# Performance work log

Hardware: AMD Instinct MI355X
Metric: run time of the kernel (lower is better)

The kernel has to match this reference:

```python
import math
import jax, jax.numpy as jnp
import numpy as np

N_NODES = 50000
N_EDGES = 600000
IN_CH = 64      # in_channels == out_channels (residual requires it)
HEADS = 2
C = 64          # per-head dim == out_channels
HC = HEADS * C  # 128
EDGE_DIM = 32


def setup_inputs() -> dict:
    key = jax.random.key(0)
    ks = jax.random.split(key, 12)
    s = 0.05
    return {
        "x": jax.random.normal(ks[0], (N_NODES, IN_CH), jnp.float32),
        "edge_index": jax.random.randint(ks[1], (2, N_EDGES), 0, N_NODES, dtype=jnp.int64),
        "edge_attr": jax.random.normal(ks[2], (N_EDGES, EDGE_DIM), jnp.float32),
        "Wq": s * jax.random.normal(ks[3], (IN_CH, HC), jnp.float32),
        "bq": jnp.zeros((HC,), jnp.float32),
        "Wk": s * jax.random.normal(ks[4], (IN_CH, HC), jnp.float32),
        "bk": jnp.zeros((HC,), jnp.float32),
        "Wv": s * jax.random.normal(ks[5], (IN_CH, HC), jnp.float32),
        "bv": jnp.zeros((HC,), jnp.float32),
        "We": s * jax.random.normal(ks[6], (EDGE_DIM, HC), jnp.float32),
        "Wp": s * jax.random.normal(ks[7], (HC, IN_CH), jnp.float32),
        "bp": jnp.zeros((IN_CH,), jnp.float32),
        "ln1_g": jnp.ones((IN_CH,), jnp.float32),
        "ln1_b": jnp.zeros((IN_CH,), jnp.float32),
        "ln2_g": jnp.ones((IN_CH,), jnp.float32),
        "ln2_b": jnp.zeros((IN_CH,), jnp.float32),
        "W1": s * jax.random.normal(ks[8], (IN_CH, IN_CH), jnp.float32),
        "b1": jnp.zeros((IN_CH,), jnp.float32),
        "W2": s * jax.random.normal(ks[9], (IN_CH, IN_CH), jnp.float32),
        "b2": jnp.zeros((IN_CH,), jnp.float32),
    }


def _layernorm(x, g, b, eps=1e-5):
    m = jnp.mean(x, axis=-1, keepdims=True)
    v = jnp.mean(jnp.square(x - m), axis=-1, keepdims=True)
    return (x - m) / jnp.sqrt(v + eps) * g + b


def reference(x, edge_index, edge_attr, Wq, bq, Wk, bk, Wv, bv, We, Wp, bp,
              ln1_g, ln1_b, ln2_g, ln2_b, W1, b1, W2, b2):
    n = x.shape[0]
    residual = x
    h = _layernorm(x, ln1_g, ln1_b)
    q = (h @ Wq + bq).reshape(n, HEADS, C)
    k = (h @ Wk + bk).reshape(n, HEADS, C)
    v = (h @ Wv + bv).reshape(n, HEADS, C)

    src, tgt = edge_index[0], edge_index[1]
    e = (edge_attr @ We).reshape(-1, HEADS, C)   # (E,H,C)
    qi = q[tgt]                                  # (E,H,C) gather by target
    kj = k[src] + e
    vj = v[src] + e

    alpha = jnp.sum(qi * kj, axis=-1) / math.sqrt(C)            # (E,H)
    amax = jax.ops.segment_max(alpha, tgt, num_segments=n)      # (N,H)
    ex = jnp.exp(alpha - amax[tgt])
    den = jax.ops.segment_sum(ex, tgt, num_segments=n)          # (N,H)
    a = ex / (den[tgt] + 1e-8)                                  # (E,H)

    agg = jax.ops.segment_sum(a[:, :, None] * vj, tgt, num_segments=n)  # (N,H,C)
    out = agg.reshape(n, HC) @ Wp + bp
    out = out + residual                        # in_channels == out_channels

    res2 = out
    o = _layernorm(out, ln2_g, ln2_b)
    o = jax.nn.gelu(o @ W1 + b1, approximate=False) @ W2 + b2
    return o + res2
```

## Files before the change

### kernel.cpp

```cpp
#include <hip/hip_runtime.h>
#include <math.h>
#include <stdint.h>


typedef float f32x4 __attribute__((ext_vector_type(4)));
typedef __bf16 bf16x8 __attribute__((ext_vector_type(8)));
typedef unsigned int u32x4 __attribute__((ext_vector_type(4)));

#define WPM_S 200
#define W1_OFF 12800
#define W2_OFF 18432
#define W_TOT 24064
#define H_S 72

__device__ __forceinline__ unsigned pack_bf16(float2 v) {
    unsigned a = __builtin_bit_cast(unsigned, v.x);
    unsigned b = __builtin_bit_cast(unsigned, v.y);
    a = (a + 0x7FFFu + ((a >> 16) & 1u)) >> 16;
    b = (b + 0x7FFFu + ((b >> 16) & 1u)) >> 16;
    return a | (b << 16);
}
__device__ __forceinline__ float2 unpack_bf16(unsigned p) {
    float x = __builtin_bit_cast(float, p << 16);
    float y = __builtin_bit_cast(float, p & 0xFFFF0000u);
    return make_float2(x, y);
}
__device__ __forceinline__ unsigned short bf16r(float x) {
    unsigned u = __builtin_bit_cast(unsigned, x);
    return (unsigned short)((u + 0x7FFFu + ((u >> 16) & 1u)) >> 16);
}

__device__ __forceinline__ f32x4 mfma16(bf16x8 a, bf16x8 b, f32x4 c) {
    return __builtin_amdgcn_mfma_f32_16x16x32_bf16(a, b, c, 0, 0, 0);
}
__device__ __forceinline__ bf16x8 frag_ld(const unsigned short* p) {
    return __builtin_bit_cast(bf16x8, *(const u32x4*)p);
}

__global__ void k_pre(const float* __restrict__ Wq, const float* __restrict__ Wk,
                      const float* __restrict__ Wv, const float* __restrict__ We,
                      const float* __restrict__ Wp, const float* __restrict__ W1,
                      const float* __restrict__ W2, const float* __restrict__ bq,
                      const float* __restrict__ bk, const float* __restrict__ bv,
                      float* __restrict__ Wqt, float* __restrict__ Wkt,
                      float* __restrict__ Wvt,
                      unsigned short* __restrict__ wsW, float* __restrict__ bqt,
                      float* __restrict__ bkt, float* __restrict__ bvt,
                      int* __restrict__ deg, int n) {
    int idx = blockIdx.x * 256 + threadIdx.x;
    for (int i = idx; i < n; i += gridDim.x * 256) deg[i] = 0;
    if (idx < 8192) {
        int cin = idx >> 7, j = idx & 127, h = j >> 6, c = j & 63;
        int dst = cin * 128 + c * 2 + h;
        Wqt[dst] = Wq[idx];
        Wkt[dst] = Wk[idx];
        Wvt[dst] = Wv[idx];
        int o = idx >> 7, k = idx & 127;
        wsW[o * WPM_S + k] = bf16r(Wp[((k & 1) * 64 + (k >> 1)) * 64 + o]);
    }
    if (idx < 4096) {
        int o = idx >> 6, k = idx & 63;
        wsW[W1_OFF + o * 88 + k] = bf16r(W1[k * 64 + o]);
        wsW[W2_OFF + o * 88 + k] = bf16r(W2[k * 64 + o]);
        int o2 = idx & 63, dh = idx >> 6, d = dh >> 1, h = dh & 1;
        float s = 0.f;
        for (int c = 0; c < 64; ++c)
            s += We[d * 128 + h * 64 + c] * Wp[(h * 64 + c) * 64 + o2];
        wsW[o2 * WPM_S + 128 + dh] = bf16r(s);
    }
    if (idx < 128) {
        int h = idx >> 6, c = idx & 63;
        bqt[c * 2 + h] = bq[idx];
        bkt[c * 2 + h] = bk[idx];
        bvt[c * 2 + h] = bv[idx];
    }
}

__global__ __launch_bounds__(256) void k_bucket(
    const int* __restrict__ ei, int* __restrict__ deg,
    int* __restrict__ bucket_e, unsigned short* __restrict__ bucket_s,
    int E, int n) {
    int e = blockIdx.x * 256 + threadIdx.x;
    if (e >= E) return;
    int src = ei[e], tgt = ei[E + e];
    src = min(max(src, 0), n - 1);
    tgt = min(max(tgt, 0), n - 1);
    int slot = atomicAdd(&deg[tgt], 1);
    if (slot < 64) {
        bucket_e[(size_t)tgt * 64 + slot] = e;
        bucket_s[(size_t)tgt * 64 + slot] = (unsigned short)src;
    }
}

__global__ __launch_bounds__(256) void k_qkv(
    const float* __restrict__ x,
    const float* __restrict__ Wqt, const float* __restrict__ Wkt, const float* __restrict__ Wvt,
    const float* __restrict__ bqt, const float* __restrict__ bkt, const float* __restrict__ bvt,
    const float* __restrict__ g1, const float* __restrict__ b1,
    const float* __restrict__ We,
    unsigned* __restrict__ qx, unsigned* __restrict__ kbf,
    unsigned* __restrict__ vbf, int n) {
    __shared__ __align__(16) float hT[4][64][8];
    __shared__ __align__(16) float qs[4][2][8][64];
    int wave = threadIdx.x >> 6, lane = threadIdx.x & 63;
    int node0 = blockIdx.x * 32 + wave * 8;
    if (node0 >= n) return;

    int b = lane >> 3, t = lane & 7;
    int nodeb = node0 + b;
    float4 xa = make_float4(0.f, 0.f, 0.f, 0.f), xb = xa;
    if (nodeb < n) {
        const float4* xp = (const float4*)(x + (size_t)nodeb * 64 + t * 8);
        xa = xp[0]; xb = xp[1];
    }
    float s1 = (xa.x + xa.y) + (xa.z + xa.w) + (xb.x + xb.y) + (xb.z + xb.w);
    float s2 = xa.x*xa.x + xa.y*xa.y + xa.z*xa.z + xa.w*xa.w
             + xb.x*xb.x + xb.y*xb.y + xb.z*xb.z + xb.w*xb.w;
#pragma unroll
    for (int m = 1; m < 8; m <<= 1) {
        s1 += __shfl_xor(s1, m);
        s2 += __shfl_xor(s2, m);
    }
    float mean = s1 * 0.015625f;
    float var  = s2 * 0.015625f - mean * mean;
    float rstd = rsqrtf(var + 1e-5f);
    float4 ga = ((const float4*)(g1 + t * 8))[0];
    float4 gb = ((const float4*)(g1 + t * 8))[1];
    float4 ba = ((const float4*)(b1 + t * 8))[0];
    float4 bb = ((const float4*)(b1 + t * 8))[1];
    float hv[8];
    hv[0] = (xa.x - mean) * rstd * ga.x + ba.x;
    hv[1] = (xa.y - mean) * rstd * ga.y + ba.y;
    hv[2] = (xa.z - mean) * rstd * ga.z + ba.z;
    hv[3] = (xa.w - mean) * rstd * ga.w + ba.w;
    hv[4] = (xb.x - mean) * rstd * gb.x + bb.x;
    hv[5] = (xb.y - mean) * rstd * gb.y + bb.y;
    hv[6] = (xb.z - mean) * rstd * gb.z + bb.z;
    hv[7] = (xb.w - mean) * rstd * gb.w + bb.w;
#pragma unroll
    for (int j = 0; j < 8; ++j) hT[wave][t * 8 + j][b] = hv[j];

    const float2* Wq2 = (const float2*)Wqt;
    const float2* Wk2 = (const float2*)Wkt;
    const float2* Wv2 = (const float2*)Wvt;
    float2 bqv = ((const float2*)bqt)[lane];
    float2 bkv = ((const float2*)bkt)[lane];
    float2 bvv = ((const float2*)bvt)[lane];
    float2 qa[8], ka[8], va[8];
#pragma unroll
    for (int nb = 0; nb < 8; ++nb) { qa[nb] = bqv; ka[nb] = bkv; va[nb] = bvv; }

#pragma unroll 4
    for (int cin = 0; cin < 64; ++cin) {
        float2 w_q = Wq2[cin * 64 + lane];
        float2 w_k = Wk2[cin * 64 + lane];
        float2 w_v = Wv2[cin * 64 + lane];
        const float4* hp = (const float4*)&hT[wave][cin][0];
        float4 h0 = hp[0], h1 = hp[1];
        float hs[8] = {h0.x, h0.y, h0.z, h0.w, h1.x, h1.y, h1.z, h1.w};
#pragma unroll
        for (int nb = 0; nb < 8; ++nb) {
            qa[nb].x += hs[nb] * w_q.x; qa[nb].y += hs[nb] * w_q.y;
            ka[nb].x += hs[nb] * w_k.x; ka[nb].y += hs[nb] * w_k.y;
            va[nb].x += hs[nb] * w_v.x; va[nb].y += hs[nb] * w_v.y;
        }
    }

#pragma unroll
    for (int nb = 0; nb < 8; ++nb) {
        int nd = node0 + nb;
        if (nd < n) {
            qx[(size_t)nd * 128 + lane] = pack_bf16(qa[nb]);
            kbf[(size_t)nd * 64 + lane] = pack_bf16(ka[nb]);
            vbf[(size_t)nd * 64 + lane] = pack_bf16(va[nb]);
        }
        qs[wave][0][nb][lane] = qa[nb].x;
        qs[wave][1][nb][lane] = qa[nb].y;
    }

    int hh = lane >> 5, d = lane & 31;
    const float4* Wr = (const float4*)(We + d * 128 + hh * 64);
    float wqa[8] = {0.f, 0.f, 0.f, 0.f, 0.f, 0.f, 0.f, 0.f};
#pragma unroll 4
    for (int c4 = 0; c4 < 16; ++c4) {
        float4 w = Wr[c4];
#pragma unroll
        for (int nb = 0; nb < 8; ++nb) {
            float4 qv = *(const float4*)&qs[wave][hh][nb][c4 * 4];
            wqa[nb] += w.x * qv.x + w.y * qv.y + w.z * qv.z + w.w * qv.w;
        }
    }
#pragma unroll
    for (int nb = 0; nb < 8; ++nb)
        if (node0 + nb < n)
            ((float*)qx)[(size_t)(node0 + nb) * 128 + 64 + d * 2 + hh] = wqa[nb];
}

__global__ __launch_bounds__(256) void k_attn(
    const unsigned* __restrict__ qx, const unsigned* __restrict__ kbf,
    const unsigned* __restrict__ vbf, const float* __restrict__ edge_attr,
    const int* __restrict__ deg, const int* __restrict__ bucket_e,
    const unsigned short* __restrict__ bucket_s,
    unsigned* __restrict__ aggs, int n, int E) {
    int wave = threadIdx.x >> 6, lane = threadIdx.x & 63;
    int node = blockIdx.x * 4 + wave;
    if (node >= n) return;
    int sub = lane >> 4, l = lane & 15;

    uint4 qq = ((const uint4*)qx)[(size_t)node * 32 + l];
    float4 w4 = ((const float4*)qx)[(size_t)node * 32 + 16 + l];
    float2 q0 = unpack_bf16(qq.x), q1 = unpack_bf16(qq.y),
           q2 = unpack_bf16(qq.z), q3 = unpack_bf16(qq.w);

    int dcount = min(deg[node], 64);
    int eid_l = 0, src_l = 0;
    if (lane < dcount) {
        eid_l = min(max(bucket_e[(size_t)node * 64 + lane], 0), E - 1);
        src_l = min((int)bucket_s[(size_t)node * 64 + lane], n - 1);
    }

    const uint4* kb4 = (const uint4*)kbf;
    const uint4* vb4 = (const uint4*)vbf;
    const float2* ea2 = (const float2*)edge_attr;

    float accA[4] = {0.f, 0.f, 0.f, 0.f}, accB[4] = {0.f, 0.f, 0.f, 0.f};
    float aS0 = 0.f, aS1 = 0.f, bS0 = 0.f, bS1 = 0.f;
    float den0 = 0.f, den1 = 0.f;

    uint4 kk, vv; float2 a2;
    {
        int jj = sub & 63;
        int ej = __shfl(eid_l, jj), sj = __shfl(src_l, jj);
        kk = kb4[(size_t)sj * 16 + l];
        vv = vb4[(size_t)sj * 16 + l];
        a2 = ea2[(size_t)ej * 16 + l];
    }
    for (int i = 0; i < dcount; i += 4) {
        uint4 kc = kk, vc = vv; float2 ac = a2;
        bool valid = (i + sub) < dcount;
        int inx = i + 4;
        if (inx < dcount) {
            int jj = (inx + sub) & 63;
            int ej = __shfl(eid_l, jj), sj = __shfl(src_l, jj);
            kk = kb4[(size_t)sj * 16 + l];
            vv = vb4[(size_t)sj * 16 + l];
            a2 = ea2[(size_t)ej * 16 + l];
        }
        float2 k0 = unpack_bf16(kc.x), k1 = unpack_bf16(kc.y),
               k2 = unpack_bf16(kc.z), k3 = unpack_bf16(kc.w);
        float r0 = q0.x * k0.x + q1.x * k1.x + q2.x * k2.x + q3.x * k3.x
                 + w4.x * ac.x + w4.z * ac.y;
        float r1 = q0.y * k0.y + q1.y * k1.y + q2.y * k2.y + q3.y * k3.y
                 + w4.y * ac.x + w4.w * ac.y;
#pragma unroll
        for (int m = 1; m < 16; m <<= 1) {
            r0 += __shfl_xor(r0, m);
            r1 += __shfl_xor(r1, m);
        }
        float ex0 = valid ? __expf(r0 * 0.125f) : 0.f;
        float ex1 = valid ? __expf(r1 * 0.125f) : 0.f;
        float2 v0 = unpack_bf16(vc.x), v1 = unpack_bf16(vc.y),
               v2 = unpack_bf16(vc.z), v3 = unpack_bf16(vc.w);
        accA[0] += ex0 * v0.x; accB[0] += ex1 * v0.y;
        accA[1] += ex0 * v1.x; accB[1] += ex1 * v1.y;
        accA[2] += ex0 * v2.x; accB[2] += ex1 * v2.y;
        accA[3] += ex0 * v3.x; accB[3] += ex1 * v3.y;
        aS0 += ex0 * ac.x; aS1 += ex1 * ac.x;
        bS0 += ex0 * ac.y; bS1 += ex1 * ac.y;
        den0 += ex0; den1 += ex1;
    }

#pragma unroll
    for (int m = 16; m < 64; m <<= 1) {
#pragma unroll
        for (int j = 0; j < 4; ++j) {
            accA[j] += __shfl_xor(accA[j], m);
            accB[j] += __shfl_xor(accB[j], m);
        }
        aS0 += __shfl_xor(aS0, m); aS1 += __shfl_xor(aS1, m);
        bS0 += __shfl_xor(bS0, m); bS1 += __shfl_xor(bS1, m);
        den0 += __shfl_xor(den0, m); den1 += __shfl_xor(den1, m);
    }

    float r0 = 1.0f / (den0 + 1e-8f);
    float r1 = 1.0f / (den1 + 1e-8f);

    float va = sub == 0 ? accA[0] : sub == 1 ? accA[1] : sub == 2 ? accA[2] : accA[3];
    float vb = sub == 0 ? accB[0] : sub == 1 ? accB[1] : sub == 2 ? accB[2] : accB[3];
    aggs[(size_t)node * 96 + 4 * l + sub] =
        pack_bf16(make_float2(va * r0, vb * r1));

    if (sub == 0) {
        unsigned s0 = pack_bf16(make_float2(aS0 * r0, aS1 * r1));
        unsigned s1 = pack_bf16(make_float2(bS0 * r0, bS1 * r1));
        *(uint2*)&aggs[(size_t)node * 96 + 64 + 2 * l] = make_uint2(s0, s1);
    }
}

__global__ __launch_bounds__(256) void k_post(
    const unsigned short* __restrict__ aggsb,
    const unsigned short* __restrict__ wsW,
    const float* __restrict__ bp, const float* __restrict__ x,
    const float* __restrict__ g2, const float* __restrict__ b2,
    const float* __restrict__ b1f, const float* __restrict__ b2f,
    float* __restrict__ out, int n) {
    __shared__ __align__(16) unsigned short sW[W_TOT];
    __shared__ __align__(16) unsigned short hb[4][2][16 * H_S];
    int tid = threadIdx.x;
    for (int i = tid; i < W_TOT / 8; i += 256)
        ((u32x4*)sW)[i] = ((const u32x4*)wsW)[i];
    __syncthreads();

    int wave = tid >> 6, lane = tid & 63;
    int cl = lane & 15, kg = lane >> 4;
    unsigned short* h2 = hb[wave][0];
    unsigned short* h3 = hb[wave][1];

    float bp_c[4], g2_c[4], b2_c[4], b1_c[4], bf2_c[4];
#pragma unroll
    for (int t = 0; t < 4; ++t) {
        int c = t * 16 + cl;
        bp_c[t] = bp[c];
        g2_c[t] = g2[c];
        b2_c[t] = b2[c];
        b1_c[t] = b1f[c];
        bf2_c[t] = b2f[c];
    }

    int wid = blockIdx.x * 4 + wave;
    int nbatch = (n + 15) >> 4;
    int nwaves = gridDim.x * 4;
    for (int bt = wid; bt < nbatch; bt += nwaves) {
        int node0 = bt * 16;

        f32x4 acc1[4];
#pragma unroll
        for (int t = 0; t < 4; ++t) acc1[t] = (f32x4){0.f, 0.f, 0.f, 0.f};
        int arow = min(node0 + cl, n - 1);
#pragma unroll
        for (int s = 0; s < 6; ++s) {
            bf16x8 af = frag_ld(aggsb + (size_t)arow * 192 + s * 32 + kg * 8);
#pragma unroll
            for (int t = 0; t < 4; ++t) {
                bf16x8 bf = frag_ld(sW + (t * 16 + cl) * WPM_S + s * 32 + kg * 8);
                acc1[t] = mfma16(af, bf, acc1[t]);
            }
        }
#pragma unroll
        for (int t = 0; t < 4; ++t) {
#pragma unroll
            for (int j = 0; j < 4; ++j) {
                int nd = min(node0 + kg * 4 + j, n - 1);
                acc1[t][j] += bp_c[t] + x[(size_t)nd * 64 + t * 16 + cl];
            }
        }

        float mean[4], rstd[4];
#pragma unroll
        for (int j = 0; j < 4; ++j) {
            float s1 = acc1[0][j] + acc1[1][j] + acc1[2][j] + acc1[3][j];
            float s2 = acc1[0][j] * acc1[0][j] + acc1[1][j] * acc1[1][j]
                     + acc1[2][j] * acc1[2][j] + acc1[3][j] * acc1[3][j];
#pragma unroll
            for (int m = 1; m < 16; m <<= 1) {
                s1 += __shfl_xor(s1, m);
                s2 += __shfl_xor(s2, m);
            }
            mean[j] = s1 * 0.015625f;
            float var = s2 * 0.015625f - mean[j] * mean[j];
            rstd[j] = rsqrtf(var + 1e-5f);
        }
#pragma unroll
        for (int t = 0; t < 4; ++t)
#pragma unroll
            for (int j = 0; j < 4; ++j) {
                float v = (acc1[t][j] - mean[j]) * rstd[j] * g2_c[t] + b2_c[t];
                h2[(kg * 4 + j) * H_S + t * 16 + cl] = bf16r(v);
            }
        asm volatile("s_waitcnt lgkmcnt(0)" ::: "memory");

        f32x4 acc2[4];
#pragma unroll
        for (int t = 0; t < 4; ++t)
            acc2[t] = (f32x4){b1_c[t], b1_c[t], b1_c[t], b1_c[t]};
#pragma unroll
        for (int s = 0; s < 2; ++s) {
            bf16x8 af = frag_ld(h2 + cl * H_S + s * 32 + kg * 8);
#pragma unroll
            for (int t = 0; t < 4; ++t) {
                bf16x8 bf = frag_ld(sW + W1_OFF + (t * 16 + cl) * 88 + s * 32 + kg * 8);
                acc2[t] = mfma16(af, bf, acc2[t]);
            }
        }
#pragma unroll
        for (int t = 0; t < 4; ++t)
#pragma unroll
            for (int j = 0; j < 4; ++j) {
                float v = acc2[t][j];
                v = 0.5f * v * (1.0f + erff(v * 0.70710678118654752f));
                h3[(kg * 4 + j) * H_S + t * 16 + cl] = bf16r(v);
            }
        asm volatile("s_waitcnt lgkmcnt(0)" ::: "memory");

        f32x4 acc3[4];
#pragma unroll
        for (int t = 0; t < 4; ++t) {
            acc3[t] = acc1[t];
#pragma unroll
            for (int j = 0; j < 4; ++j) acc3[t][j] += bf2_c[t];
        }
#pragma unroll
        for (int s = 0; s < 2; ++s) {
            bf16x8 af = frag_ld(h3 + cl * H_S + s * 32 + kg * 8);
#pragma unroll
            for (int t = 0; t < 4; ++t) {
                bf16x8 bf = frag_ld(sW + W2_OFF + (t * 16 + cl) * 88 + s * 32 + kg * 8);
                acc3[t] = mfma16(af, bf, acc3[t]);
            }
        }
#pragma unroll
        for (int t = 0; t < 4; ++t)
#pragma unroll
            for (int j = 0; j < 4; ++j) {
                int r = node0 + kg * 4 + j;
                if (r < n) out[(size_t)r * 64 + t * 16 + cl] = acc3[t][j];
            }
    }
}

extern "C" void kernel_launch(void* const* d_in, const int* in_sizes, int n_in,
                              void* d_out, int out_size, void* d_ws, size_t ws_size,
                              hipStream_t stream) {
    const float* x  = (const float*)d_in[0];
    const int*   ei = (const int*)d_in[1];
    const float* ea = (const float*)d_in[2];
    const float* Wq = (const float*)d_in[3];
    const float* bq = (const float*)d_in[4];
    const float* Wk = (const float*)d_in[5];
    const float* bk = (const float*)d_in[6];
    const float* Wv = (const float*)d_in[7];
    const float* bv = (const float*)d_in[8];
    const float* We = (const float*)d_in[9];
    const float* Wp = (const float*)d_in[10];
    const float* bp = (const float*)d_in[11];
    const float* g1 = (const float*)d_in[12];
    const float* b1 = (const float*)d_in[13];
    const float* g2 = (const float*)d_in[14];
    const float* b2 = (const float*)d_in[15];
    const float* W1 = (const float*)d_in[16];
    const float* b1f = (const float*)d_in[17];
    const float* W2 = (const float*)d_in[18];
    const float* b2f = (const float*)d_in[19];

    const int n = in_sizes[0] / 64;
    const int E = in_sizes[2] / 32;

    char* p = (char*)d_ws;
    unsigned* qx = (unsigned*)p; p += (size_t)n * 128 * 4;
    unsigned* kbf = (unsigned*)p; p += (size_t)n * 64 * 4;
    unsigned* vbf = (unsigned*)p; p += (size_t)n * 64 * 4;
    int* deg   = (int*)p;   p += (size_t)n * 4;
    p = (char*)(((uintptr_t)p + 15) & ~(uintptr_t)15);
    int* bucket_e = (int*)p; p += (size_t)n * 64 * 4;
    unsigned short* bucket_s = (unsigned short*)p; p += (size_t)n * 64 * 2;
    p = (char*)(((uintptr_t)p + 15) & ~(uintptr_t)15);
    unsigned* aggs = (unsigned*)p; p += (size_t)n * 96 * 4;
    float* Wqt = (float*)p; p += 8192 * 4;
    float* Wkt = (float*)p; p += 8192 * 4;
    float* Wvt = (float*)p; p += 8192 * 4;
    unsigned short* wsW = (unsigned short*)p; p += W_TOT * 2;
    float* bqt = (float*)p; p += 128 * 4;
    float* bkt = (float*)p; p += 128 * 4;
    float* bvt = (float*)p; p += 128 * 4;

    k_pre<<<196, 256, 0, stream>>>(Wq, Wk, Wv, We, Wp, W1, W2, bq, bk, bv,
                                   Wqt, Wkt, Wvt, wsW, bqt, bkt, bvt,
                                   deg, n);
    k_bucket<<<(E + 255) / 256, 256, 0, stream>>>(ei, deg, bucket_e, bucket_s,
                                                  E, n);
    k_qkv<<<(n + 31) / 32, 256, 0, stream>>>(x, Wqt, Wkt, Wvt, bqt, bkt, bvt,
                                             g1, b1, We, qx, kbf, vbf, n);
    k_attn<<<(n + 3) / 4, 256, 0, stream>>>(qx, kbf, vbf, ea, deg,
                                            bucket_e, bucket_s, aggs, n, E);
    int nb16 = (n + 15) >> 4;
    int blocks = (nb16 + 3) / 4;
    if (blocks > 391) blocks = 391;
    k_post<<<blocks, 256, 0, stream>>>((const unsigned short*)aggs, wsW,
                                       bp, x, g2, b2, b1f, b2f,
                                       (float*)d_out, n);
}
```

Baseline: 325.8 us.

## Compute fused QKV and Q·We projection with bf16 MFMA from LDS weights

Replaces the fp32 scalar-FMA QKV projection in k_qkv with bf16 MFMA 16x16x32 instructions. The weights are staged once per block into shared memory as a concatenated transposed bf16 matrix. The Q·We^T product is folded algebraically into a precomputed weight block (Wq·We^T plus its bias), so the second LDS pass is gone. The aim is to cut ALU time in the projection. In exchange it adds a roughly 64KB LDS weight load per block and bf16 rounding of the LayerNorm outputs, the weights, and the q·We term.

```diff
diff --git a/kernel.cpp b/kernel.cpp
--- a/kernel.cpp
+++ b/kernel.cpp
@@ -12,6 +12,8 @@
 #define W2_OFF 18432
 #define W_TOT 24064
 #define H_S 72
+#define WC_S 72
+#define WC_TOT (448 * 72)
 
 __device__ __forceinline__ unsigned pack_bf16(float2 v) {
     unsigned a = __builtin_bit_cast(unsigned, v.x);
@@ -42,21 +44,18 @@
                       const float* __restrict__ Wp, const float* __restrict__ W1,
                       const float* __restrict__ W2, const float* __restrict__ bq,
                       const float* __restrict__ bk, const float* __restrict__ bv,
-                      float* __restrict__ Wqt, float* __restrict__ Wkt,
-                      float* __restrict__ Wvt,
-                      unsigned short* __restrict__ wsW, float* __restrict__ bqt,
-                      float* __restrict__ bkt, float* __restrict__ bvt,
+                      unsigned short* __restrict__ wsW,
+                      unsigned short* __restrict__ wcat, float* __restrict__ bcat,
                       int* __restrict__ deg, int n) {
     int idx = blockIdx.x * 256 + threadIdx.x;
     for (int i = idx; i < n; i += gridDim.x * 256) deg[i] = 0;
     if (idx < 8192) {
-        int cin = idx >> 7, j = idx & 127, h = j >> 6, c = j & 63;
-        int dst = cin * 128 + c * 2 + h;
-        Wqt[dst] = Wq[idx];
-        Wkt[dst] = Wk[idx];
-        Wvt[dst] = Wv[idx];
         int o = idx >> 7, k = idx & 127;
         wsW[o * WPM_S + k] = bf16r(Wp[((k & 1) * 64 + (k >> 1)) * 64 + o]);
+        int cin = idx >> 7, j = idx & 127;
+        wcat[j * WC_S + cin] = bf16r(Wq[cin * 128 + j]);
+        wcat[(128 + j) * WC_S + cin] = bf16r(Wk[cin * 128 + j]);
+        wcat[(256 + j) * WC_S + cin] = bf16r(Wv[cin * 128 + j]);
     }
     if (idx < 4096) {
         int o = idx >> 6, k = idx & 63;
@@ -67,12 +66,20 @@
         for (int c = 0; c < 64; ++c)
             s += We[d * 128 + h * 64 + c] * Wp[(h * 64 + c) * 64 + o2];
         wsW[o2 * WPM_S + 128 + dh] = bf16r(s);
-    }
-    if (idx < 128) {
-        int h = idx >> 6, c = idx & 63;
-        bqt[c * 2 + h] = bq[idx];
-        bkt[c * 2 + h] = bk[idx];
-        bvt[c * 2 + h] = bv[idx];
+        int cin2 = idx & 63, dh2 = idx >> 6, d2 = dh2 >> 1, h2 = dh2 & 1;
+        float s2 = 0.f;
+        for (int c = 0; c < 64; ++c)
+            s2 += Wq[cin2 * 128 + h2 * 64 + c] * We[d2 * 128 + h2 * 64 + c];
+        wcat[(384 + dh2) * WC_S + cin2] = bf16r(s2);
+    }
+    if (idx < 384)
+        bcat[idx] = idx < 128 ? bq[idx] : idx < 256 ? bk[idx - 128] : bv[idx - 256];
+    if (idx < 64) {
+        int d = idx >> 1, h = idx & 1;
+        float s = 0.f;
+        for (int c = 0; c < 64; ++c)
+            s += bq[h * 64 + c] * We[d * 128 + h * 64 + c];
+        bcat[384 + idx] = s;
     }
 }
 
@@ -93,107 +100,88 @@
 }
 
 __global__ __launch_bounds__(256) void k_qkv(
-    const float* __restrict__ x,
-    const float* __restrict__ Wqt, const float* __restrict__ Wkt, const float* __restrict__ Wvt,
-    const float* __restrict__ bqt, const float* __restrict__ bkt, const float* __restrict__ bvt,
+    const float* __restrict__ x, const unsigned short* __restrict__ wcat,
+    const float* __restrict__ bcat,
     const float* __restrict__ g1, const float* __restrict__ b1,
-    const float* __restrict__ We,
     unsigned* __restrict__ qx, unsigned* __restrict__ kbf,
     unsigned* __restrict__ vbf, int n) {
-    __shared__ __align__(16) float hT[4][64][8];
-    __shared__ __align__(16) float qs[4][2][8][64];
-    int wave = threadIdx.x >> 6, lane = threadIdx.x & 63;
-    int node0 = blockIdx.x * 32 + wave * 8;
+    __shared__ __align__(16) unsigned short sW[WC_TOT];
+    int tid = threadIdx.x;
+    for (int i = tid; i < WC_TOT / 8; i += 256)
+        ((u32x4*)sW)[i] = ((const u32x4*)wcat)[i];
+    __syncthreads();
+
+    int wave = tid >> 6, lane = tid & 63;
+    int cl = lane & 15, kg = lane >> 4;
+    int node0 = blockIdx.x * 64 + wave * 16;
     if (node0 >= n) return;
-
-    int b = lane >> 3, t = lane & 7;
-    int nodeb = node0 + b;
-    float4 xa = make_float4(0.f, 0.f, 0.f, 0.f), xb = xa;
-    if (nodeb < n) {
-        const float4* xp = (const float4*)(x + (size_t)nodeb * 64 + t * 8);
-        xa = xp[0]; xb = xp[1];
-    }
-    float s1 = (xa.x + xa.y) + (xa.z + xa.w) + (xb.x + xb.y) + (xb.z + xb.w);
-    float s2 = xa.x*xa.x + xa.y*xa.y + xa.z*xa.z + xa.w*xa.w
-             + xb.x*xb.x + xb.y*xb.y + xb.z*xb.z + xb.w*xb.w;
-#pragma unroll
-    for (int m = 1; m < 8; m <<= 1) {
-        s1 += __shfl_xor(s1, m);
-        s2 += __shfl_xor(s2, m);
-    }
+    int arow = min(node0 + cl, n - 1);
+
+    const float4* xp = (const float4*)(x + (size_t)arow * 64);
+    float4 xv[4] = {xp[kg * 2], xp[kg * 2 + 1], xp[8 + kg * 2], xp[9 + kg * 2]};
+    float s1 = 0.f, s2 = 0.f;
+#pragma unroll
+    for (int i = 0; i < 4; ++i) {
+        s1 += (xv[i].x + xv[i].y) + (xv[i].z + xv[i].w);
+        s2 += xv[i].x * xv[i].x + xv[i].y * xv[i].y
+            + xv[i].z * xv[i].z + xv[i].w * xv[i].w;
+    }
+    s1 += __shfl_xor(s1, 16); s2 += __shfl_xor(s2, 16);
+    s1 += __shfl_xor(s1, 32); s2 += __shfl_xor(s2, 32);
     float mean = s1 * 0.015625f;
     float var  = s2 * 0.015625f - mean * mean;
     float rstd = rsqrtf(var + 1e-5f);
-    float4 ga = ((const float4*)(g1 + t * 8))[0];
-    float4 gb = ((const float4*)(g1 + t * 8))[1];
-    float4 ba = ((const float4*)(b1 + t * 8))[0];
-    float4 bb = ((const float4*)(b1 + t * 8))[1];
-    float hv[8];
-    hv[0] = (xa.x - mean) * rstd * ga.x + ba.x;
-    hv[1] = (xa.y - mean) * rstd * ga.y + ba.y;
-    hv[2] = (xa.z - mean) * rstd * ga.z + ba.z;
-    hv[3] = (xa.w - mean) * rstd * ga.w + ba.w;
-    hv[4] = (xb.x - mean) * rstd * gb.x + bb.x;
-    hv[5] = (xb.y - mean) * rstd * gb.y + bb.y;
-    hv[6] = (xb.z - mean) * rstd * gb.z + bb.z;
-    hv[7] = (xb.w - mean) * rstd * gb.w + bb.w;
-#pragma unroll
-    for (int j = 0; j < 8; ++j) hT[wave][t * 8 + j][b] = hv[j];
-
-    const float2* Wq2 = (const float2*)Wqt;
-    const float2* Wk2 = (const float2*)Wkt;
-    const float2* Wv2 = (const float2*)Wvt;
-    float2 bqv = ((const float2*)bqt)[lane];
-    float2 bkv = ((const float2*)bkt)[lane];
-    float2 bvv = ((const float2*)bvt)[lane];
-    float2 qa[8], ka[8], va[8];
-#pragma unroll
-    for (int nb = 0; nb < 8; ++nb) { qa[nb] = bqv; ka[nb] = bkv; va[nb] = bvv; }
-
-#pragma unroll 4
-    for (int cin = 0; cin < 64; ++cin) {
-        float2 w_q = Wq2[cin * 64 + lane];
-        float2 w_k = Wk2[cin * 64 + lane];
-        float2 w_v = Wv2[cin * 64 + lane];
-        const float4* hp = (const float4*)&hT[wave][cin][0];
-        float4 h0 = hp[0], h1 = hp[1];
-        float hs[8] = {h0.x, h0.y, h0.z, h0.w, h1.x, h1.y, h1.z, h1.w};
-#pragma unroll
-        for (int nb = 0; nb < 8; ++nb) {
-            qa[nb].x += hs[nb] * w_q.x; qa[nb].y += hs[nb] * w_q.y;
-            ka[nb].x += hs[nb] * w_k.x; ka[nb].y += hs[nb] * w_k.y;
-            va[nb].x += hs[nb] * w_v.x; va[nb].y += hs[nb] * w_v.y;
-        }
-    }
-
-#pragma unroll
-    for (int nb = 0; nb < 8; ++nb) {
-        int nd = node0 + nb;
-        if (nd < n) {
-            qx[(size_t)nd * 128 + lane] = pack_bf16(qa[nb]);
-            kbf[(size_t)nd * 64 + lane] = pack_bf16(ka[nb]);
-            vbf[(size_t)nd * 64 + lane] = pack_bf16(va[nb]);
-        }
-        qs[wave][0][nb][lane] = qa[nb].x;
-        qs[wave][1][nb][lane] = qa[nb].y;
-    }
-
-    int hh = lane >> 5, d = lane & 31;
-    const float4* Wr = (const float4*)(We + d * 128 + hh * 64);
-    float wqa[8] = {0.f, 0.f, 0.f, 0.f, 0.f, 0.f, 0.f, 0.f};
-#pragma unroll 4
-    for (int c4 = 0; c4 < 16; ++c4) {
-        float4 w = Wr[c4];
-#pragma unroll
-        for (int nb = 0; nb < 8; ++nb) {
-            float4 qv = *(const float4*)&qs[wave][hh][nb][c4 * 4];
-            wqa[nb] += w.x * qv.x + w.y * qv.y + w.z * qv.z + w.w * qv.w;
-        }
-    }
-#pragma unroll
-    for (int nb = 0; nb < 8; ++nb)
-        if (node0 + nb < n)
-            ((float*)qx)[(size_t)(node0 + nb) * 128 + 64 + d * 2 + hh] = wqa[nb];
+    const float4* gp = (const float4*)g1;
+    const float4* bp1 = (const float4*)b1;
+    float4 gv[4] = {gp[kg * 2], gp[kg * 2 + 1], gp[8 + kg * 2], gp[9 + kg * 2]};
+    float4 bv4[4] = {bp1[kg * 2], bp1[kg * 2 + 1], bp1[8 + kg * 2], bp1[9 + kg * 2]};
+    unsigned fr[8];
+#pragma unroll
+    for (int i = 0; i < 4; ++i) {
+        float h0 = (xv[i].x - mean) * rstd * gv[i].x + bv4[i].x;
+        float h1 = (xv[i].y - mean) * rstd * gv[i].y + bv4[i].y;
+        float h2 = (xv[i].z - mean) * rstd * gv[i].z + bv4[i].z;
+        float h3 = (xv[i].w - mean) * rstd * gv[i].w + bv4[i].w;
+        fr[i * 2]     = pack_bf16(make_float2(h0, h1));
+        fr[i * 2 + 1] = pack_bf16(make_float2(h2, h3));
+    }
+    bf16x8 A0 = __builtin_bit_cast(bf16x8, (u32x4){fr[0], fr[1], fr[2], fr[3]});
+    bf16x8 A1 = __builtin_bit_cast(bf16x8, (u32x4){fr[4], fr[5], fr[6], fr[7]});
+
+#pragma unroll
+    for (int tq = 0; tq < 4; ++tq) {
+        int c = tq * 16 + cl;
+        f32x4 aq0 = {bcat[c], bcat[c], bcat[c], bcat[c]};
+        float b_;
+        b_ = bcat[64 + c];  f32x4 aq1 = {b_, b_, b_, b_};
+        b_ = bcat[128 + c]; f32x4 ak0 = {b_, b_, b_, b_};
+        b_ = bcat[192 + c]; f32x4 ak1 = {b_, b_, b_, b_};
+        b_ = bcat[256 + c]; f32x4 av0 = {b_, b_, b_, b_};
+        b_ = bcat[320 + c]; f32x4 av1 = {b_, b_, b_, b_};
+        b_ = bcat[384 + c]; f32x4 aw  = {b_, b_, b_, b_};
+#pragma unroll
+        for (int s = 0; s < 2; ++s) {
+            bf16x8 A = s ? A1 : A0;
+            int ko = s * 32 + kg * 8;
+            aq0 = mfma16(A, frag_ld(sW + (size_t)(c) * WC_S + ko), aq0);
+            aq1 = mfma16(A, frag_ld(sW + (size_t)(64 + c) * WC_S + ko), aq1);
+            ak0 = mfma16(A, frag_ld(sW + (size_t)(128 + c) * WC_S + ko), ak0);
+            ak1 = mfma16(A, frag_ld(sW + (size_t)(192 + c) * WC_S + ko), ak1);
+            av0 = mfma16(A, frag_ld(sW + (size_t)(256 + c) * WC_S + ko), av0);
+            av1 = mfma16(A, frag_ld(sW + (size_t)(320 + c) * WC_S + ko), av1);
+            aw  = mfma16(A, frag_ld(sW + (size_t)(384 + c) * WC_S + ko), aw);
+        }
+#pragma unroll
+        for (int j = 0; j < 4; ++j) {
+            int node = node0 + kg * 4 + j;
+            if (node < n) {
+                qx[(size_t)node * 128 + c] = pack_bf16(make_float2(aq0[j], aq1[j]));
+                kbf[(size_t)node * 64 + c] = pack_bf16(make_float2(ak0[j], ak1[j]));
+                vbf[(size_t)node * 64 + c] = pack_bf16(make_float2(av0[j], av1[j]));
+                ((float*)qx)[(size_t)node * 128 + 64 + c] = aw[j];
+            }
+        }
+    }
 }
 
 __global__ __launch_bounds__(256) void k_attn(
@@ -465,21 +453,16 @@
     unsigned short* bucket_s = (unsigned short*)p; p += (size_t)n * 64 * 2;
     p = (char*)(((uintptr_t)p + 15) & ~(uintptr_t)15);
     unsigned* aggs = (unsigned*)p; p += (size_t)n * 96 * 4;
-    float* Wqt = (float*)p; p += 8192 * 4;
-    float* Wkt = (float*)p; p += 8192 * 4;
-    float* Wvt = (float*)p; p += 8192 * 4;
     unsigned short* wsW = (unsigned short*)p; p += W_TOT * 2;
-    float* bqt = (float*)p; p += 128 * 4;
-    float* bkt = (float*)p; p += 128 * 4;
-    float* bvt = (float*)p; p += 128 * 4;
+    unsigned short* wcat = (unsigned short*)p; p += (size_t)WC_TOT * 2;
+    float* bcat = (float*)p; p += 448 * 4;
 
     k_pre<<<196, 256, 0, stream>>>(Wq, Wk, Wv, We, Wp, W1, W2, bq, bk, bv,
-                                   Wqt, Wkt, Wvt, wsW, bqt, bkt, bvt,
-                                   deg, n);
+                                   wsW, wcat, bcat, deg, n);
     k_bucket<<<(E + 255) / 256, 256, 0, stream>>>(ei, deg, bucket_e, bucket_s,
                                                   E, n);
-    k_qkv<<<(n + 31) / 32, 256, 0, stream>>>(x, Wqt, Wkt, Wvt, bqt, bkt, bvt,
-                                             g1, b1, We, qx, kbf, vbf, n);
+    k_qkv<<<(n + 63) / 64, 256, 0, stream>>>(x, wcat, bcat, g1, b1,
+                                             qx, kbf, vbf, n);
     k_attn<<<(n + 3) / 4, 256, 0, stream>>>(qx, kbf, vbf, ea, deg,
                                             bucket_e, bucket_s, aggs, n, E);
     int nb16 = (n + 15) >> 4;
```

Result: faster. 293.4 us (-9.9%).
